# Optimization experiments

Measured on AMD Instinct MI355X. Metric: run time of the kernel, lower is better.

## Reference

```python
import jax, jax.numpy as jnp
import numpy as np

B, CIN, D, H, W = 2, 64, 64, 64, 64
NUM_CLASSES = 5
STRIDE = 2
NMAX = 32
TOPK = 13
TAL_ALPHA, TAL_BETA = 1.0, 6.0
EPS = 1e-9


def setup_inputs() -> dict:
    key = jax.random.key(0)
    ks = jax.random.split(key, 6)
    features = jax.random.normal(ks[0], (B, CIN, D, H, W), jnp.float32)
    cls_w = jax.random.normal(ks[1], (NUM_CLASSES, CIN, 3, 3, 3), jnp.float32) * 0.02
    cls_b = jnp.zeros((NUM_CLASSES,), jnp.float32)
    off_w = jax.random.normal(ks[2], (3, CIN, 3, 3, 3), jnp.float32) * 0.01
    off_b = jnp.zeros((3,), jnp.float32)
    coords = jax.random.uniform(ks[3], (B, NMAX, 3), jnp.float32, 4.0, float(D * STRIDE) - 4.0)
    cls = jax.random.randint(ks[4], (B, NMAX, 1), 0, NUM_CLASSES).astype(jnp.float32)
    sigma = jax.random.uniform(ks[5], (B, NMAX, 1), jnp.float32, 2.0, 8.0)
    pad = (jnp.arange(NMAX) >= 24)[None, :, None]  # last 8 GT slots are padding
    cls = jnp.where(pad, -100.0, cls)
    labels = jnp.concatenate([coords, cls, sigma], axis=-1)  # B N 5 : x,y,z,class,sigma
    return {"features": features, "cls_w": cls_w, "cls_b": cls_b,
            "off_w": off_w, "off_b": off_b, "labels": labels}


def conv3d(x, w, b):
    y = jax.lax.conv_general_dilated(x, w, (1, 1, 1), 'SAME',
                                     dimension_numbers=('NCDHW', 'OIDHW', 'NCDHW'))
    return y + b[None, :, None, None, None]


def make_anchors():
    g = jnp.stack(jnp.meshgrid(jnp.arange(D), jnp.arange(H), jnp.arange(W), indexing='ij'))
    return (g.astype(jnp.float32) + 0.5) * STRIDE  # (3, D, H, W)


def flatten_bchw(x):
    # B C D H W -> B (D H W) C
    Bsz, C = x.shape[0], x.shape[1]
    return x.transpose(0, 2, 3, 4, 1).reshape(Bsz, -1, C)


def tal_assign(pred_logits, pred_centers, true_labels, true_centers, true_sigmas, valid):
    # pred_logits (B,L,C); pred_centers (B,L,3); true_* (B,N,...); valid (B,N) bool
    Bsz, L, C = pred_logits.shape
    N = true_labels.shape[1]
    d2 = jnp.sum((true_centers[:, :, None, :] - pred_centers[:, None, :, :]) ** 2, -1)  # B N L
    ious = jnp.exp(-d2 / (2.0 * true_sigmas[:, :, None] ** 2))  # keypoint IoU, B N L
    probs = jax.nn.sigmoid(pred_logits).transpose(0, 2, 1)  # B C L
    cls_scores = jnp.take_along_axis(probs, true_labels[:, :, None], axis=1)  # B N L
    align = (cls_scores ** TAL_ALPHA) * (ious ** TAL_BETA)  # alignment metric
    topv, topi = jax.lax.top_k(align, TOPK)
    is_topk = jnp.zeros_like(align).at[
        jnp.arange(Bsz)[:, None, None], jnp.arange(N)[None, :, None], topi
    ].set(jnp.where(topv > EPS, 1.0, 0.0))
    mask_pos = is_topk * valid[:, :, None].astype(align.dtype)  # B N L
    pos_sum = mask_pos.sum(axis=1)  # B L
    # resolve anchors matched to multiple GTs: keep GT with max IoU
    is_max_iou = jax.nn.one_hot(jnp.argmax(ious, axis=1), N, axis=1, dtype=align.dtype)
    mask_pos = jnp.where(pos_sum[:, None, :] > 1, is_max_iou, mask_pos)
    pos_sum = mask_pos.sum(axis=1)
    fg = pos_sum > 0  # B L
    assigned_gt = jnp.argmax(mask_pos, axis=1)  # B L
    assigned_labels = jnp.take_along_axis(true_labels, assigned_gt, axis=1)
    assigned_labels = jnp.where(fg, assigned_labels, C)  # bg_index = C
    assigned_centers = jnp.take_along_axis(true_centers, assigned_gt[:, :, None], axis=1)  # B L 3
    assigned_sigmas = jnp.take_along_axis(true_sigmas, assigned_gt, axis=1)  # B L
    align = align * mask_pos
    max_align = align.max(axis=2, keepdims=True)  # B N 1
    max_iou = (ious * mask_pos).max(axis=2, keepdims=True)
    score = (align * max_iou / (max_align + EPS)).max(axis=1)  # B L
    assigned_scores = jax.nn.one_hot(assigned_labels, C + 1)[..., :C] * score[..., None]  # B L C
    return assigned_labels, assigned_centers, assigned_scores, assigned_sigmas


def detection_loss(logits, offsets, anchors, labels):
    pred_logits = flatten_bchw(logits)               # B L C
    pred_centers = flatten_bchw(anchors + offsets)   # B L 3
    anchor_pts = flatten_bchw(anchors)
    C = pred_logits.shape[-1]
    true_centers = labels[..., :3]
    true_labels_f = labels[..., 3]
    true_sigmas = labels[..., 4]
    valid = true_labels_f != -100.0
    true_labels = jnp.where(valid, true_labels_f, 0.0).astype(jnp.int32)
    assigned = tal_assign(jax.lax.stop_gradient(pred_logits),
                          jax.lax.stop_gradient(pred_centers),
                          true_labels, true_centers, true_sigmas, valid)
    assigned_labels, assigned_centers, assigned_scores, assigned_sigmas = jax.lax.stop_gradient(assigned)
    one_hot_label = jax.nn.one_hot(assigned_labels, C + 1)[..., :C]
    # varifocal loss (alpha=0.75, gamma=2)
    p = jax.nn.sigmoid(pred_logits)
    weight = 0.75 * (p ** 2.0) * (1.0 - one_hot_label) + assigned_scores * one_hot_label
    bce = assigned_scores * jax.nn.softplus(-pred_logits) + (1.0 - assigned_scores) * jax.nn.softplus(pred_logits)
    cls_loss = jnp.sum(weight * bce)
    d = jnp.sum((pred_centers - assigned_centers) ** 2, -1)  # B L
    w = assigned_scores.sum(-1)
    iou = jnp.exp(-d / (2.0 * assigned_sigmas ** 2))
    mask_positive = assigned_labels != C
    reg_loss = jnp.sum(jnp.where(mask_positive, (1.0 - iou) * w, 0.0))
    return (cls_loss + reg_loss) / assigned_scores.sum()


def reference(features, cls_w, cls_b, off_w, off_b, labels):
    logits = conv3d(features, cls_w, cls_b)    # B C D H W
    offsets = conv3d(features, off_w, off_b)   # B 3 D H W
    anchors = jnp.broadcast_to(make_anchors()[None], (features.shape[0], 3, D, H, W))
    loss = detection_loss(logits, offsets, anchors, labels)
    return loss
```

## Files before the change

kernel.cpp:

```cpp
#include <hip/hip_runtime.h>
#include <math.h>

#define NB 2
#define CIN 64
#define DD_ 64
#define HH_ 64
#define WW_ 64
#define NCLS 5
#define LL (DD_*HH_*WW_)
#define NMAXG 32
#define TOPKK 13
#define SEG 16
#define SEGL (LL/SEG)

typedef __attribute__((ext_vector_type(8))) short short8b;
typedef __attribute__((ext_vector_type(4))) float floatx4;

__device__ __forceinline__ float softplusf_(float z){
  return fmaxf(z, 0.f) + log1pf(expf(-fabsf(z)));
}
__device__ __forceinline__ float sigmoidf_(float z){
  return 1.f/(1.f + expf(-z));
}
__device__ __forceinline__ unsigned tobf_u_(float f){
  unsigned u = __float_as_uint(f);
  return (u + 0x7fffu + ((u>>16)&1u)) >> 16;
}
__device__ __forceinline__ short tobf_(float f){
  return (short)tobf_u_(f);
}

__global__ __launch_bounds__(256) void wtrans_kernel(
    const float* __restrict__ cls_w, const float* __restrict__ off_w,
    short* __restrict__ wA)
{
  int idx = blockIdx.x*256 + threadIdx.x;
  if (idx >= 72*64) return;
  int slice = idx >> 6; int lane = idx & 63;
  int cc = slice & 3; int r = slice >> 2;
  int s  = r & 1;     int kk = r >> 1;
  int kd = kk/3, kw = kk - 3*(kk/3);
  int m = lane & 15, g = lane >> 4;
  short8b out;
  #pragma unroll
  for (int i=0;i<8;++i){
    int k = g*8 + i; int khl = k >> 4; int cl = k & 15;
    int kh = (s==0) ? khl : (khl==0 ? 2 : -1);
    float wv = 0.f;
    if (m < 8 && kh >= 0){
      int c = cc*16 + cl;
      if (m < NCLS) wv = cls_w[(m*CIN + c)*27 + (kd*3+kh)*3 + kw];
      else          wv = off_w[((m-NCLS)*CIN + c)*27 + (kd*3+kh)*3 + kw];
    }
    out[i] = tobf_(wv);
  }
  *(short8b*)(wA + (size_t)idx*8) = out;
}

__global__ __launch_bounds__(512, 4) void conv_mfma_kernel(
    const float* __restrict__ feat,
    const short* __restrict__ wA,
    const float* __restrict__ cls_b, const float* __restrict__ off_b,
    float* __restrict__ logits_ws,
    float* __restrict__ centers_ws,
    float* __restrict__ bg_sum)
{
  __shared__ short xs[36*68*16];
  __shared__ float bsum[8];

  const int tid = threadIdx.x;
  const int lane = tid & 63, wv = tid >> 6;
  const int col = lane & 15, g = lane >> 4;
  const int chalf = g & 1, khl = g >> 1;
  const int h0 = blockIdx.x*4, d0 = blockIdx.y*4, b = blockIdx.z;

  for (int idx = tid; idx < 36*32; idx += 512){
    int row = idx >> 5; int rr = idx & 31;
    int wp = (rr < 16) ? 0 : 65;
    xs[(row*68 + wp)*16 + (rr & 15)] = 0;
  }

  floatx4 acc[8];
  #pragma unroll
  for (int t=0;t<8;++t) acc[t] = (floatx4){0.f,0.f,0.f,0.f};

  const short8b* wAv = (const short8b*)wA;

  for (int cc=0; cc<4; ++cc){
    if (cc) __syncthreads();
    #pragma unroll 1
    for (int it=0; it<9; ++it){
      int idx = it*512 + tid;
      int p   = idx / 576;
      int rem = idx - p*576;
      int row = rem >> 4;
      int w4  = rem & 15;
      int row_d = row/6;
      int row_h = row - row_d*6;
      int d_ = d0 - 1 + row_d;
      int h_ = h0 - 1 + row_h;
      float4 x0 = make_float4(0.f,0.f,0.f,0.f);
      float4 x1 = x0;
      if (d_ >= 0 && d_ < DD_ && h_ >= 0 && h_ < HH_){
        const float* pp = feat + ((((size_t)b*CIN + cc*16 + 2*p)*DD_ + d_)*HH_ + h_)*WW_ + w4*4;
        x0 = *(const float4*)pp;
        x1 = *(const float4*)(pp + LL);
      }
      int base = row*68*16 + ((2*p)&7);
      int swp  = p>>2;
      #pragma unroll
      for (int j=0;j<4;++j){
        int wp = w4*4 + j + 1;
        float a0 = (j==0)?x0.x:((j==1)?x0.y:((j==2)?x0.z:x0.w));
        float a1 = (j==0)?x1.x:((j==1)?x1.y:((j==2)?x1.z:x1.w));
        unsigned pk = (tobf_u_(a1)<<16) | tobf_u_(a0);
        int sw = swp ^ ((wp>>2)&1);
        *(unsigned*)(xs + base + wp*16 + (sw<<3)) = pk;
      }
    }
    __syncthreads();
    #pragma unroll 1
    for (int kk=0; kk<9; ++kk){
      int kd = kk/3, kw = kk - 3*(kd);
      #pragma unroll
      for (int s=0;s<2;++s){
        int slice = (kk*2 + s)*4 + cc;
        short8b a = wAv[slice*64 + lane];
        int khe = s ? 2 : khl;
        #pragma unroll
        for (int t=0;t<8;++t){
          int tile = wv*8 + t;
          int dl = tile>>4, hl = (tile>>2)&3, wq = tile&3;
          int row = (dl+kd)*6 + hl + khe;
          int wp = wq*16 + col + kw;
          int sidx = (row*68 + wp)*16 + ((chalf ^ ((wp>>2)&1))<<3);
          short8b bfr = *(const short8b*)(xs + sidx);
          acc[t] = __builtin_amdgcn_mfma_f32_16x16x32_bf16(a, bfr, acc[t], 0,0,0);
        }
      }
    }
  }

  float bg = 0.f;
  #pragma unroll
  for (int t=0;t<8;++t){
    int tile = wv*8 + t;
    int dl = tile>>4, hl = (tile>>2)&3, wq = tile&3;
    int d = d0+dl, h = h0+hl, w = wq*16 + col;
    size_t l = (size_t)d*4096 + (size_t)h*64 + w;
    if (g == 0){
      #pragma unroll
      for (int j=0;j<4;++j){
        float z = acc[t][j] + cls_b[j];
        logits_ws[(size_t)(b*NCLS+j)*LL + l] = z;
        float pr = sigmoidf_(z);
        bg += 0.75f*pr*pr*softplusf_(z);
      }
    } else if (g == 1){
      float z = acc[t][0] + cls_b[4];
      logits_ws[(size_t)(b*NCLS+4)*LL + l] = z;
      float pr = sigmoidf_(z);
      bg += 0.75f*pr*pr*softplusf_(z);
      float4 ctr;
      ctr.x = ((float)d+0.5f)*2.f + acc[t][1] + off_b[0];
      ctr.y = ((float)h+0.5f)*2.f + acc[t][2] + off_b[1];
      ctr.z = ((float)w+0.5f)*2.f + acc[t][3] + off_b[2];
      ctr.w = 0.f;
      *(float4*)(centers_ws + ((size_t)b*LL + l)*4) = ctr;
    }
  }
  #pragma unroll
  for (int off=32;off;off>>=1) bg += __shfl_down(bg, off);
  if (lane == 0) bsum[wv] = bg;
  __syncthreads();
  if (tid == 0){
    float s = 0.f;
    #pragma unroll
    for (int i=0;i<8;++i) s += bsum[i];
    atomicAdd(bg_sum, s);
  }
}

__global__ __launch_bounds__(256) void topk_partial_kernel(
    const float* __restrict__ logits_ws, const float* __restrict__ centers_ws,
    const float* __restrict__ labels,
    float* __restrict__ pv, int* __restrict__ pi)
{
  const int bn = blockIdx.x;
  const int seg = blockIdx.y;
  const int b = bn >> 5, n = bn & 31;
  const int tid = threadIdx.x;

  const float* lb = labels + (b*NMAXG + n)*5;
  const float tx = lb[0], ty = lb[1], tz = lb[2];
  const float cf = lb[3];
  const float sg = lb[4];
  const int lab = (cf == -100.f) ? 0 : (int)cf;
  const float m6 = -3.f/(sg*sg);

  const float* lg = logits_ws + (size_t)(b*NCLS + lab)*LL;
  const float* cb = centers_ws + (size_t)b*LL*4;

  float v[13]; int ix[13];
  #pragma unroll
  for (int j=0;j<13;++j){ v[j]=-1.f; ix[j]=0x7fffffff; }

  const int l0 = seg*SEGL;
  for (int l = l0 + tid; l < l0 + SEGL; l += 256){
    float4 c4 = *(const float4*)(cb + (size_t)l*4);
    float dx = c4.x-tx, dy = c4.y-ty, dz = c4.z-tz;
    float e = m6*(dx*dx + dy*dy + dz*dz);
    if (e < -20.8f) continue;
    float a = sigmoidf_(lg[l]) * expf(e);
    if (a > v[12]){
      float cv = a; int ci = l;
      #pragma unroll
      for (int j=0;j<13;++j){
        bool take = (cv > v[j]) || (cv == v[j] && ci < ix[j]);
        float nv = take ? cv : v[j];  float ov = take ? v[j] : cv;
        int   ni = take ? ci : ix[j]; int   oi = take ? ix[j] : ci;
        v[j]=nv; ix[j]=ni; cv=ov; ci=oi;
      }
    }
  }

  const int lane = tid & 63, wvi = tid >> 6;
  float mv = -2.f; int mi = 0x7fffffff;
  #pragma unroll 1
  for (int k=0;k<13;++k){
    float bv = v[0]; int bi = ix[0]; int bl = lane;
    #pragma unroll
    for (int off=32; off; off>>=1){
      float ov2 = __shfl_xor(bv, off);
      int oi = __shfl_xor(bi, off);
      int ol = __shfl_xor(bl, off);
      if (ov2 > bv || (ov2 == bv && oi < bi)){ bv=ov2; bi=oi; bl=ol; }
    }
    if (lane == k){ mv = bv; mi = bi; }
    if (lane == bl){
      #pragma unroll
      for (int j=0;j<12;++j){ v[j]=v[j+1]; ix[j]=ix[j+1]; }
      v[12] = -2.f; ix[12] = 0x7fffffff;
    }
  }
  __shared__ float sv2[4*13]; __shared__ int si2[4*13];
  if (lane < 13){ sv2[wvi*13+lane] = mv; si2[wvi*13+lane] = mi; }
  __syncthreads();
  if (wvi == 0){
    float v2 = -2.f; int i2 = 0x7fffffff;
    if (lane < 52){ v2 = sv2[lane]; i2 = si2[lane]; }
    #pragma unroll 1
    for (int k=0;k<13;++k){
      float bv = v2; int bi = i2; int bl = lane;
      #pragma unroll
      for (int off=32; off; off>>=1){
        float ov2 = __shfl_xor(bv, off);
        int oi = __shfl_xor(bi, off);
        int ol = __shfl_xor(bl, off);
        if (ov2 > bv || (ov2 == bv && oi < bi)){ bv=ov2; bi=oi; bl=ol; }
      }
      if (lane == 0){
        pv[(bn*SEG+seg)*TOPKK + k] = bv;
        pi[(bn*SEG+seg)*TOPKK + k] = bi;
      }
      if (lane == bl) v2 = -2.f;
    }
  }
}

__global__ __launch_bounds__(256) void topk_merge_kernel(
    const float* __restrict__ pv, const int* __restrict__ pi,
    float* __restrict__ tv, int* __restrict__ ti)
{
  const int bn = blockIdx.x;
  const int t = threadIdx.x;
  const int NC = SEG*TOPKK;
  float v = -2.f; int ix = 0x7fffffff;
  if (t < NC){ v = pv[bn*NC + t]; ix = pi[bn*NC + t]; }
  __shared__ float sv[256]; __shared__ int si[256]; __shared__ int sl[256];
  for (int k=0;k<13;++k){
    sv[t]=v; si[t]=ix; sl[t]=t;
    __syncthreads();
    for (int s2=128;s2;s2>>=1){
      if (t<s2){
        if (sv[t+s2]>sv[t] || (sv[t+s2]==sv[t] && si[t+s2]<si[t])){
          sv[t]=sv[t+s2]; si[t]=si[t+s2]; sl[t]=sl[t+s2];
        }
      }
      __syncthreads();
    }
    if (t==0){ tv[bn*TOPKK+k]=sv[0]; ti[bn*TOPKK+k]=si[0]; }
    int win = sl[0];
    __syncthreads();
    if (t==win) v = -2.f;
  }
}

__global__ __launch_bounds__(512) void finalize_kernel(
    const float* __restrict__ logits_ws, const float* __restrict__ centers_ws,
    const float* __restrict__ labels,
    const float* __restrict__ tv, const int* __restrict__ ti,
    const float* __restrict__ bg_sum, float* __restrict__ out)
{
  const int tid = threadIdx.x;
  __shared__ float gx[32], gy[32], gz[32], gs[32];
  __shared__ int glab[32], gvalid[32];
  __shared__ int hkey[1024], hcnt[1024], hmin[1024];
  __shared__ unsigned maxA[32], maxI[32];
  __shared__ float accD, accC;
  if (tid==0){ accD=0.f; accC=0.f; }

  for (int b=0;b<NB;++b){
    for (int i=tid;i<1024;i+=512){ hkey[i]=-1; hcnt[i]=0; hmin[i]=0x7fffffff; }
    if (tid<32){
      const float* lb = labels + (b*NMAXG + tid)*5;
      gx[tid]=lb[0]; gy[tid]=lb[1]; gz[tid]=lb[2];
      float cf = lb[3]; gs[tid]=lb[4];
      int val = (cf != -100.f);
      gvalid[tid]=val; glab[tid]= val ? (int)cf : 0;
      maxA[tid]=0u; maxI[tid]=0u;
    }
    __syncthreads();

    const int e = tid;
    bool ok = false; int l = -1; int n = 0;
    if (e < 416){
      n = e/13; int k = e - 13*n;
      float v = tv[(b*NMAXG+n)*TOPKK + k];
      l = ti[(b*NMAXG+n)*TOPKK + k];
      ok = gvalid[n] && (v > 1e-9f);
    }
    int slot = -1;
    if (ok){
      unsigned h = (((unsigned)l * 2654435761u) >> 20) & 1023u;
      for (;;){
        int prev = atomicCAS(&hkey[h], -1, l);
        if (prev == -1 || prev == l){ slot = (int)h; break; }
        h = (h+1) & 1023u;
      }
      atomicAdd(&hcnt[slot], 1);
      atomicMin(&hmin[slot], e);
    }
    __syncthreads();

    bool first = ok && (hmin[slot] == e);
    float a=0.f, iou=0.f; int nstar=0;
    if (first){
      float px = centers_ws[((size_t)b*LL + l)*4 + 0];
      float py = centers_ws[((size_t)b*LL + l)*4 + 1];
      float pz = centers_ws[((size_t)b*LL + l)*4 + 2];
      if (hcnt[slot] == 1){
        nstar = n;
      } else {
        float best = -1.f; int bidx = 0;
        for (int nn=0;nn<32;++nn){
          float dx=gx[nn]-px, dy=gy[nn]-py, dz=gz[nn]-pz;
          float d2 = dx*dx+dy*dy+dz*dz;
          float io = expf(-d2/(2.f*gs[nn]*gs[nn]));
          if (io > best){ best=io; bidx=nn; }
        }
        nstar = bidx;
      }
      float dx=gx[nstar]-px, dy=gy[nstar]-py, dz=gz[nstar]-pz;
      float d2 = dx*dx+dy*dy+dz*dz;
      float sgv = gs[nstar];
      iou = expf(-d2/(2.f*sgv*sgv));
      float z = logits_ws[(size_t)(b*NCLS + glab[nstar])*LL + l];
      a = sigmoidf_(z) * expf(-3.f*d2/(sgv*sgv));
      atomicMax(&maxA[nstar], __float_as_uint(a));
      atomicMax(&maxI[nstar], __float_as_uint(iou));
    }
    __syncthreads();

    if (first){
      float mA = __uint_as_float(maxA[nstar]);
      float mI = __uint_as_float(maxI[nstar]);
      float score = a*mI/(mA + 1e-9f);
      float z = logits_ws[(size_t)(b*NCLS + glab[nstar])*LL + l];
      float p = sigmoidf_(z);
      float t2 = log1pf(expf(-fabsf(z)));
      float spz = fmaxf(z,0.f) + t2;
      float spm = fmaxf(-z,0.f) + t2;
      float corr = score*(score*spm + (1.f-score)*spz) - 0.75f*p*p*spz;
      float reg  = (1.f - iou)*score;
      atomicAdd(&accD, score);
      atomicAdd(&accC, corr + reg);
    }
    __syncthreads();
  }
  if (tid==0) out[0] = (bg_sum[0] + accC) / accD;
}

extern "C" void kernel_launch(void* const* d_in, const int* in_sizes, int n_in,
                              void* d_out, int out_size, void* d_ws, size_t ws_size,
                              hipStream_t stream) {
  const float* feat  = (const float*)d_in[0];
  const float* cls_w = (const float*)d_in[1];
  const float* cls_b = (const float*)d_in[2];
  const float* off_w = (const float*)d_in[3];
  const float* off_b = (const float*)d_in[4];
  const float* labels= (const float*)d_in[5];
  float* out = (float*)d_out;

  float* logits_ws  = (float*)d_ws;
  float* centers_ws = logits_ws + (size_t)NB*NCLS*LL;
  float* pv = centers_ws + (size_t)NB*LL*4;
  int*   pi = (int*)(pv + 64*SEG*TOPKK);
  float* tv = (float*)(pi + 64*SEG*TOPKK);
  int*   ti = (int*)(tv + 64*TOPKK);
  float* bg = (float*)(ti + 64*TOPKK);
  short* wA = (short*)(bg + 16);

  hipMemsetAsync(bg, 0, sizeof(float), stream);

  wtrans_kernel<<<18, 256, 0, stream>>>(cls_w, off_w, wA);
  conv_mfma_kernel<<<dim3(16,16,2), 512, 0, stream>>>(
      feat, wA, cls_b, off_b, logits_ws, centers_ws, bg);
  topk_partial_kernel<<<dim3(64,SEG), 256, 0, stream>>>(
      logits_ws, centers_ws, labels, pv, pi);
  topk_merge_kernel<<<64, 256, 0, stream>>>(pv, pi, tv, ti);
  finalize_kernel<<<1, 512, 0, stream>>>(
      logits_ws, centers_ws, labels, tv, ti, bg, out);
}
```

Measured before the change: 202.7 us.

## Restrict top-k search to bounding box per GT and repack conv MFMA over depth pairs

The conv kernel now records the maximum absolute predicted offset through an atomicMax. The top-k kernel uses that value to scan only anchors inside a conservative box around each ground-truth center, where the alignment could exceed the cutoff. This replaces the full-volume scan over 16 segments and removes the separate merge kernel. The conv weights are also repacked so one MFMA covers two depth slices (rows 8-15 hold kd-shifted weights), halving accumulators per wave, and feature staging now writes 8 channels per uint4 store. The box radius depends on the exp cutoff, so correctness relies on that bound; a single block per GT may also give low parallelism if boxes are large.

```diff
diff --git a/kernel.cpp b/kernel.cpp
--- a/kernel.cpp
+++ b/kernel.cpp
@@ -10,8 +10,6 @@
 #define LL (DD_*HH_*WW_)
 #define NMAXG 32
 #define TOPKK 13
-#define SEG 16
-#define SEGL (LL/SEG)
 
 typedef __attribute__((ext_vector_type(8))) short short8b;
 typedef __attribute__((ext_vector_type(4))) float floatx4;
@@ -35,22 +33,24 @@
     short* __restrict__ wA)
 {
   int idx = blockIdx.x*256 + threadIdx.x;
-  if (idx >= 72*64) return;
+  if (idx >= 96*64) return;
   int slice = idx >> 6; int lane = idx & 63;
-  int cc = slice & 3; int r = slice >> 2;
-  int s  = r & 1;     int kk = r >> 1;
-  int kd = kk/3, kw = kk - 3*(kk/3);
+  int cc = slice & 3; int r2 = slice >> 2;
+  int kw = r2 - 3*(r2/3); int r3 = r2/3;
+  int s  = r3 & 1;        int rr = r3 >> 1;
   int m = lane & 15, g = lane >> 4;
+  int outch = m & 7;
+  int kd = (m < 8) ? rr : rr - 1;
   short8b out;
   #pragma unroll
   for (int i=0;i<8;++i){
     int k = g*8 + i; int khl = k >> 4; int cl = k & 15;
     int kh = (s==0) ? khl : (khl==0 ? 2 : -1);
     float wv = 0.f;
-    if (m < 8 && kh >= 0){
+    if (kd >= 0 && kd <= 2 && kh >= 0){
       int c = cc*16 + cl;
-      if (m < NCLS) wv = cls_w[(m*CIN + c)*27 + (kd*3+kh)*3 + kw];
-      else          wv = off_w[((m-NCLS)*CIN + c)*27 + (kd*3+kh)*3 + kw];
+      if (outch < NCLS) wv = cls_w[(outch*CIN + c)*27 + (kd*3+kh)*3 + kw];
+      else              wv = off_w[((outch-NCLS)*CIN + c)*27 + (kd*3+kh)*3 + kw];
     }
     out[i] = tobf_(wv);
   }
@@ -63,7 +63,8 @@
     const float* __restrict__ cls_b, const float* __restrict__ off_b,
     float* __restrict__ logits_ws,
     float* __restrict__ centers_ws,
-    float* __restrict__ bg_sum)
+    float* __restrict__ bg_sum,
+    unsigned* __restrict__ moff_u)
 {
   __shared__ short xs[36*68*16];
   __shared__ float bsum[8];
@@ -75,14 +76,14 @@
   const int h0 = blockIdx.x*4, d0 = blockIdx.y*4, b = blockIdx.z;
 
   for (int idx = tid; idx < 36*32; idx += 512){
-    int row = idx >> 5; int rr = idx & 31;
-    int wp = (rr < 16) ? 0 : 65;
-    xs[(row*68 + wp)*16 + (rr & 15)] = 0;
-  }
-
-  floatx4 acc[8];
+    int row = idx >> 5; int rr2 = idx & 31;
+    int wp = (rr2 < 16) ? 0 : 65;
+    xs[(row*68 + wp)*16 + (rr2 & 15)] = 0;
+  }
+
+  floatx4 acc[4];
   #pragma unroll
-  for (int t=0;t<8;++t) acc[t] = (floatx4){0.f,0.f,0.f,0.f};
+  for (int t=0;t<4;++t) acc[t] = (floatx4){0.f,0.f,0.f,0.f};
 
   const short8b* wAv = (const short8b*)wA;
 
@@ -91,64 +92,60 @@
     #pragma unroll 1
     for (int it=0; it<9; ++it){
       int idx = it*512 + tid;
-      int p   = idx / 576;
-      int rem = idx - p*576;
-      int row = rem >> 4;
-      int w4  = rem & 15;
+      int half = idx & 1;
+      int wp1  = ((idx>>1) & 63) + 1;
+      int row  = idx >> 7;
       int row_d = row/6;
       int row_h = row - row_d*6;
       int d_ = d0 - 1 + row_d;
       int h_ = h0 - 1 + row_h;
-      float4 x0 = make_float4(0.f,0.f,0.f,0.f);
-      float4 x1 = x0;
-      if (d_ >= 0 && d_ < DD_ && h_ >= 0 && h_ < HH_){
-        const float* pp = feat + ((((size_t)b*CIN + cc*16 + 2*p)*DD_ + d_)*HH_ + h_)*WW_ + w4*4;
-        x0 = *(const float4*)pp;
-        x1 = *(const float4*)(pp + LL);
-      }
-      int base = row*68*16 + ((2*p)&7);
-      int swp  = p>>2;
-      #pragma unroll
-      for (int j=0;j<4;++j){
-        int wp = w4*4 + j + 1;
-        float a0 = (j==0)?x0.x:((j==1)?x0.y:((j==2)?x0.z:x0.w));
-        float a1 = (j==0)?x1.x:((j==1)?x1.y:((j==2)?x1.z:x1.w));
-        unsigned pk = (tobf_u_(a1)<<16) | tobf_u_(a0);
-        int sw = swp ^ ((wp>>2)&1);
-        *(unsigned*)(xs + base + wp*16 + (sw<<3)) = pk;
-      }
+      bool inb = (d_>=0 && d_<DD_ && h_>=0 && h_<HH_);
+      const float* pp = feat + ((((size_t)b*CIN + cc*16 + half*8)*DD_ + (inb?d_:0))*HH_ + (inb?h_:0))*WW_ + (wp1-1);
+      float f[8];
+      #pragma unroll
+      for (int j=0;j<8;++j) f[j] = inb ? pp[(size_t)j*LL] : 0.f;
+      uint4 pk;
+      pk.x = (tobf_u_(f[1])<<16) | tobf_u_(f[0]);
+      pk.y = (tobf_u_(f[3])<<16) | tobf_u_(f[2]);
+      pk.z = (tobf_u_(f[5])<<16) | tobf_u_(f[4]);
+      pk.w = (tobf_u_(f[7])<<16) | tobf_u_(f[6]);
+      int off = (row*68 + wp1)*16 + ((half ^ ((wp1>>2)&1))<<3);
+      *(uint4*)(xs + off) = pk;
     }
     __syncthreads();
     #pragma unroll 1
-    for (int kk=0; kk<9; ++kk){
-      int kd = kk/3, kw = kk - 3*(kd);
+    for (int rr=0; rr<4; ++rr){
       #pragma unroll
       for (int s=0;s<2;++s){
-        int slice = (kk*2 + s)*4 + cc;
-        short8b a = wAv[slice*64 + lane];
-        int khe = s ? 2 : khl;
         #pragma unroll
-        for (int t=0;t<8;++t){
-          int tile = wv*8 + t;
-          int dl = tile>>4, hl = (tile>>2)&3, wq = tile&3;
-          int row = (dl+kd)*6 + hl + khe;
-          int wp = wq*16 + col + kw;
-          int sidx = (row*68 + wp)*16 + ((chalf ^ ((wp>>2)&1))<<3);
-          short8b bfr = *(const short8b*)(xs + sidx);
-          acc[t] = __builtin_amdgcn_mfma_f32_16x16x32_bf16(a, bfr, acc[t], 0,0,0);
+        for (int kw=0;kw<3;++kw){
+          int slice = ((rr*2+s)*3+kw)*4+cc;
+          short8b a = wAv[slice*64 + lane];
+          int khe = s ? 2 : khl;
+          #pragma unroll
+          for (int t=0;t<4;++t){
+            int tile = wv*4 + t;
+            int dp = tile>>4, hl = (tile>>2)&3, wq = tile&3;
+            int row = (2*dp + rr)*6 + hl + khe;
+            int wp = wq*16 + col + kw;
+            int sidx = (row*68 + wp)*16 + ((chalf ^ ((wp>>2)&1))<<3);
+            short8b bfr = *(const short8b*)(xs + sidx);
+            acc[t] = __builtin_amdgcn_mfma_f32_16x16x32_bf16(a, bfr, acc[t], 0,0,0);
+          }
         }
       }
     }
   }
 
   float bg = 0.f;
+  float om = 0.f;
   #pragma unroll
-  for (int t=0;t<8;++t){
-    int tile = wv*8 + t;
-    int dl = tile>>4, hl = (tile>>2)&3, wq = tile&3;
-    int d = d0+dl, h = h0+hl, w = wq*16 + col;
+  for (int t=0;t<4;++t){
+    int tile = wv*4 + t;
+    int dp = tile>>4, hl = (tile>>2)&3, wq = tile&3;
+    int d = d0 + 2*dp + (g>>1), h = h0+hl, w = wq*16 + col;
     size_t l = (size_t)d*4096 + (size_t)h*64 + w;
-    if (g == 0){
+    if ((g&1) == 0){
       #pragma unroll
       for (int j=0;j<4;++j){
         float z = acc[t][j] + cls_b[j];
@@ -156,22 +153,32 @@
         float pr = sigmoidf_(z);
         bg += 0.75f*pr*pr*softplusf_(z);
       }
-    } else if (g == 1){
+    } else {
       float z = acc[t][0] + cls_b[4];
       logits_ws[(size_t)(b*NCLS+4)*LL + l] = z;
       float pr = sigmoidf_(z);
       bg += 0.75f*pr*pr*softplusf_(z);
+      float o0 = acc[t][1] + off_b[0];
+      float o1 = acc[t][2] + off_b[1];
+      float o2 = acc[t][3] + off_b[2];
+      om = fmaxf(om, fmaxf(fabsf(o0), fmaxf(fabsf(o1), fabsf(o2))));
       float4 ctr;
-      ctr.x = ((float)d+0.5f)*2.f + acc[t][1] + off_b[0];
-      ctr.y = ((float)h+0.5f)*2.f + acc[t][2] + off_b[1];
-      ctr.z = ((float)w+0.5f)*2.f + acc[t][3] + off_b[2];
+      ctr.x = ((float)d+0.5f)*2.f + o0;
+      ctr.y = ((float)h+0.5f)*2.f + o1;
+      ctr.z = ((float)w+0.5f)*2.f + o2;
       ctr.w = 0.f;
       *(float4*)(centers_ws + ((size_t)b*LL + l)*4) = ctr;
     }
   }
   #pragma unroll
-  for (int off=32;off;off>>=1) bg += __shfl_down(bg, off);
-  if (lane == 0) bsum[wv] = bg;
+  for (int off=32;off;off>>=1){
+    bg += __shfl_down(bg, off);
+    om = fmaxf(om, __shfl_xor(om, off));
+  }
+  if (lane == 0){
+    bsum[wv] = bg;
+    atomicMax(moff_u, __float_as_uint(om));
+  }
   __syncthreads();
   if (tid == 0){
     float s = 0.f;
@@ -181,13 +188,13 @@
   }
 }
 
-__global__ __launch_bounds__(256) void topk_partial_kernel(
+__global__ __launch_bounds__(256) void topk_box_kernel(
     const float* __restrict__ logits_ws, const float* __restrict__ centers_ws,
     const float* __restrict__ labels,
-    float* __restrict__ pv, int* __restrict__ pi)
+    const unsigned* __restrict__ moff_u,
+    float* __restrict__ tv, int* __restrict__ ti)
 {
   const int bn = blockIdx.x;
-  const int seg = blockIdx.y;
   const int b = bn >> 5, n = bn & 31;
   const int tid = threadIdx.x;
 
@@ -197,6 +204,17 @@
   const float sg = lb[4];
   const int lab = (cf == -100.f) ? 0 : (int)cf;
   const float m6 = -3.f/(sg*sg);
+  const float moff = __uint_as_float(*moff_u);
+  const float R = 2.6336f*sg + moff + 0.05f;
+
+  int i0d = (int)ceilf((tx - R - 1.f)*0.5f); if (i0d < 0) i0d = 0;
+  int i1d = (int)floorf((tx + R - 1.f)*0.5f); if (i1d > 63) i1d = 63;
+  int i0h = (int)ceilf((ty - R - 1.f)*0.5f); if (i0h < 0) i0h = 0;
+  int i1h = (int)floorf((ty + R - 1.f)*0.5f); if (i1h > 63) i1h = 63;
+  int i0w = (int)ceilf((tz - R - 1.f)*0.5f); if (i0w < 0) i0w = 0;
+  int i1w = (int)floorf((tz + R - 1.f)*0.5f); if (i1w > 63) i1w = 63;
+  int nd = i1d-i0d+1, nh = i1h-i0h+1, nw = i1w-i0w+1;
+  int total = (nd>0 && nh>0 && nw>0) ? nd*nh*nw : 0;
 
   const float* lg = logits_ws + (size_t)(b*NCLS + lab)*LL;
   const float* cb = centers_ws + (size_t)b*LL*4;
@@ -205,8 +223,11 @@
   #pragma unroll
   for (int j=0;j<13;++j){ v[j]=-1.f; ix[j]=0x7fffffff; }
 
-  const int l0 = seg*SEGL;
-  for (int l = l0 + tid; l < l0 + SEGL; l += 256){
+  for (int idx = tid; idx < total; idx += 256){
+    int r = idx;
+    int wi = r % nw; r /= nw;
+    int hi = r % nh; int di = r / nh;
+    int l = (i0d+di)*4096 + (i0h+hi)*64 + (i0w+wi);
     float4 c4 = *(const float4*)(cb + (size_t)l*4);
     float dx = c4.x-tx, dy = c4.y-ty, dz = c4.z-tz;
     float e = m6*(dx*dx + dy*dy + dz*dz);
@@ -260,39 +281,11 @@
         if (ov2 > bv || (ov2 == bv && oi < bi)){ bv=ov2; bi=oi; bl=ol; }
       }
       if (lane == 0){
-        pv[(bn*SEG+seg)*TOPKK + k] = bv;
-        pi[(bn*SEG+seg)*TOPKK + k] = bi;
+        tv[bn*TOPKK + k] = bv;
+        ti[bn*TOPKK + k] = bi;
       }
       if (lane == bl) v2 = -2.f;
     }
-  }
-}
-
-__global__ __launch_bounds__(256) void topk_merge_kernel(
-    const float* __restrict__ pv, const int* __restrict__ pi,
-    float* __restrict__ tv, int* __restrict__ ti)
-{
-  const int bn = blockIdx.x;
-  const int t = threadIdx.x;
-  const int NC = SEG*TOPKK;
-  float v = -2.f; int ix = 0x7fffffff;
-  if (t < NC){ v = pv[bn*NC + t]; ix = pi[bn*NC + t]; }
-  __shared__ float sv[256]; __shared__ int si[256]; __shared__ int sl[256];
-  for (int k=0;k<13;++k){
-    sv[t]=v; si[t]=ix; sl[t]=t;
-    __syncthreads();
-    for (int s2=128;s2;s2>>=1){
-      if (t<s2){
-        if (sv[t+s2]>sv[t] || (sv[t+s2]==sv[t] && si[t+s2]<si[t])){
-          sv[t]=sv[t+s2]; si[t]=si[t+s2]; sl[t]=sl[t+s2];
-        }
-      }
-      __syncthreads();
-    }
-    if (t==0){ tv[bn*TOPKK+k]=sv[0]; ti[bn*TOPKK+k]=si[0]; }
-    int win = sl[0];
-    __syncthreads();
-    if (t==win) v = -2.f;
   }
 }
 
@@ -404,21 +397,18 @@
 
   float* logits_ws  = (float*)d_ws;
   float* centers_ws = logits_ws + (size_t)NB*NCLS*LL;
-  float* pv = centers_ws + (size_t)NB*LL*4;
-  int*   pi = (int*)(pv + 64*SEG*TOPKK);
-  float* tv = (float*)(pi + 64*SEG*TOPKK);
+  float* tv = centers_ws + (size_t)NB*LL*4;
   int*   ti = (int*)(tv + 64*TOPKK);
   float* bg = (float*)(ti + 64*TOPKK);
   short* wA = (short*)(bg + 16);
 
-  hipMemsetAsync(bg, 0, sizeof(float), stream);
-
-  wtrans_kernel<<<18, 256, 0, stream>>>(cls_w, off_w, wA);
+  hipMemsetAsync(bg, 0, 8, stream);
+
+  wtrans_kernel<<<24, 256, 0, stream>>>(cls_w, off_w, wA);
   conv_mfma_kernel<<<dim3(16,16,2), 512, 0, stream>>>(
-      feat, wA, cls_b, off_b, logits_ws, centers_ws, bg);
-  topk_partial_kernel<<<dim3(64,SEG), 256, 0, stream>>>(
-      logits_ws, centers_ws, labels, pv, pi);
-  topk_merge_kernel<<<64, 256, 0, stream>>>(pv, pi, tv, ti);
+      feat, wA, cls_b, off_b, logits_ws, centers_ws, bg, (unsigned*)(bg+1));
+  topk_box_kernel<<<64, 256, 0, stream>>>(
+      logits_ws, centers_ws, labels, (const unsigned*)(bg+1), tv, ti);
   finalize_kernel<<<1, 512, 0, stream>>>(
       logits_ws, centers_ws, labels, tv, ti, bg, out);
 }
```

Result: slower. 213.0 us (+5.1%).
